# Kernel tuning notes

Measured on AMD Instinct MI355X. Metric: run time of the kernel, lower is better.

## Reference

```python
import jax, jax.numpy as jnp
import numpy as np

B, S, HID, NH = 64, 197, 768, 12
DH = HID // NH  # 64
EPS = 1e-24


def setup_inputs() -> dict:
    key = jax.random.key(0)
    ks = jax.random.split(key, 20)
    def lin(i):
        w = jax.random.normal(ks[i], (HID, HID), jnp.float32) * 0.02  # stored [in, out]
        b = jnp.zeros((HID,), jnp.float32)
        return w, b
    Wmq, bmq = lin(0); Wcq, bcq = lin(1)
    Wmk, bmk = lin(2); Wck, bck = lin(3)
    Wmv, bmv = lin(4); Wcv, bcv = lin(5)
    Wmd, bmd = lin(6); Wcd, bcd = lin(7)
    return dict(
        input_mean_tensor=jax.random.normal(ks[8], (B, S, HID), jnp.float32),
        input_cov_tensor=jax.random.normal(ks[9], (B, S, HID), jnp.float32),
        Wmq=Wmq, bmq=bmq, Wcq=Wcq, bcq=bcq,
        Wmk=Wmk, bmk=bmk, Wck=Wck, bck=bck,
        Wmv=Wmv, bmv=bmv, Wcv=Wcv, bcv=bcv,
        Wmd=Wmd, bmd=bmd, Wcd=Wcd, bcd=bcd,
    )


def _heads(x):
    # [B, S, HID] -> [B, NH, S, DH]
    return x.reshape(x.shape[0], x.shape[1], NH, DH).transpose(0, 2, 1, 3)


def _merge(x):
    # [B, NH, S, DH] -> [B, S, HID]
    return x.transpose(0, 2, 1, 3).reshape(x.shape[0], x.shape[2], HID)


def wasserstein_distance_matmul(m1, c1, m2, c2):
    # all [B, NH, S, DH]; returns [B, NH, S, S]
    m1_2 = jnp.sum(m1 * m1, -1, keepdims=True)            # [B,NH,S,1]
    m2_2 = jnp.sum(m2 * m2, -1, keepdims=True)
    ret = m1_2 + jnp.swapaxes(m2_2, -1, -2) - 2.0 * jnp.einsum('bhqd,bhkd->bhqk', m1, m2)
    c1_2 = jnp.sum(c1, -1, keepdims=True)
    c2_2 = jnp.sum(c2, -1, keepdims=True)
    s1 = jnp.sqrt(jnp.clip(c1, EPS, None))
    s2 = jnp.sqrt(jnp.clip(c2, EPS, None))
    cov_ret = c1_2 + jnp.swapaxes(c2_2, -1, -2) - 2.0 * jnp.einsum('bhqd,bhkd->bhqk', s1, s2)
    return ret + cov_ret


def reference(input_mean_tensor, input_cov_tensor,
              Wmq, bmq, Wcq, bcq, Wmk, bmk, Wck, bck,
              Wmv, bmv, Wcv, bcv, Wmd, bmd, Wcd, bcd):
    mean_q = _heads(input_mean_tensor @ Wmq + bmq)
    mean_k = _heads(input_mean_tensor @ Wmk + bmk)
    mean_v = _heads(input_mean_tensor @ Wmv + bmv)
    cov_q = _heads(jax.nn.elu(input_cov_tensor @ Wcq + bcq) + 1.0)
    cov_k = _heads(jax.nn.elu(input_cov_tensor @ Wck + bck) + 1.0)
    cov_v = _heads(jax.nn.elu(input_cov_tensor @ Wcv + bcv) + 1.0)

    scores = -wasserstein_distance_matmul(mean_q, cov_q, mean_k, cov_k)
    scores = scores / jnp.sqrt(jnp.float32(DH))
    probs = jax.nn.softmax(scores, axis=-1)  # [B,NH,S,S]

    mean_ctx = _merge(jnp.einsum('bhqk,bhkd->bhqd', probs, mean_v))
    cov_ctx = _merge(jnp.einsum('bhqk,bhkd->bhqd', probs * probs, cov_v))

    mean_hidden = mean_ctx @ Wmd + bmd
    cov_hidden = cov_ctx @ Wcd + bcd
    return (mean_hidden, cov_hidden)
```

## Files before the change

### kernel.cpp

```cpp
#include <hip/hip_runtime.h>
#include <hip/hip_bf16.h>
#include <stdint.h>

typedef _Float16 f16;
typedef _Float16 f16x8 __attribute__((ext_vector_type(8)));
typedef _Float16 f16x4 __attribute__((ext_vector_type(4)));
typedef float f32x4 __attribute__((ext_vector_type(4)));

constexpr int B = 64, S = 197, HID = 768, NH = 12, DH = 64;
constexpr int M = B * S;
constexpr int Mpad = 12800;
constexpr int BNS = B * NH * S;
constexpr int VSTRIDE = 224;
constexpr size_t NPH = (size_t)Mpad * HID;
constexpr size_t MH = (size_t)M * HID;
constexpr size_t WSZ1 = (size_t)HID * HID;
constexpr size_t VTSZ = (size_t)B * NH * DH * VSTRIDE;

__device__ __forceinline__ f32x4 mfma16(f16x8 a, f16x8 b, f32x4 c) {
  return __builtin_amdgcn_mfma_f32_16x16x32_f16(a, b, c, 0, 0, 0);
}

__device__ __forceinline__ void gload16(const void* g, void* l) {
  __builtin_amdgcn_global_load_lds(
      (const __attribute__((address_space(1))) void*)g,
      (__attribute__((address_space(3))) void*)l, 16, 0, 0);
}

__device__ __forceinline__ int xcd_swizzle(int wg, int nwg) {
  const int q = nwg >> 3, r = nwg & 7;
  const int x = wg & 7, p = wg >> 3;
  return (x < r ? x * (q + 1) : r * (q + 1) + (x - r) * q) + p;
}

__global__ __launch_bounds__(256) void zero_kernel(char* __restrict__ p, size_t n16) {
  const size_t i = (size_t)blockIdx.x * 256 + threadIdx.x;
  if (i < n16) reinterpret_cast<int4*>(p)[i] = int4{0, 0, 0, 0};
}

__global__ __launch_bounds__(256) void cvt_x_kernel(
    const float* __restrict__ xm, const float* __restrict__ xc,
    f16* __restrict__ ym, f16* __restrict__ yc) {
  const size_t i8 = ((size_t)blockIdx.x * 256 + threadIdx.x) * 8;
  f16x8 vm = {}, vc = {};
  if (i8 < MH) {
    const float4 a0 = *reinterpret_cast<const float4*>(xm + i8);
    const float4 a1 = *reinterpret_cast<const float4*>(xm + i8 + 4);
    const float4 b0 = *reinterpret_cast<const float4*>(xc + i8);
    const float4 b1 = *reinterpret_cast<const float4*>(xc + i8 + 4);
    vm[0] = (f16)a0.x; vm[1] = (f16)a0.y; vm[2] = (f16)a0.z; vm[3] = (f16)a0.w;
    vm[4] = (f16)a1.x; vm[5] = (f16)a1.y; vm[6] = (f16)a1.z; vm[7] = (f16)a1.w;
    vc[0] = (f16)b0.x; vc[1] = (f16)b0.y; vc[2] = (f16)b0.z; vc[3] = (f16)b0.w;
    vc[4] = (f16)b1.x; vc[5] = (f16)b1.y; vc[6] = (f16)b1.z; vc[7] = (f16)b1.w;
  }
  *reinterpret_cast<f16x8*>(ym + i8) = vm;
  *reinterpret_cast<f16x8*>(yc + i8) = vc;
}

struct WPtrs { const float* w[8]; };

__global__ __launch_bounds__(256) void cvt_w_kernel(WPtrs p, f16* __restrict__ wt) {
  __shared__ float tile[32][33];
  const int z = blockIdx.z;
  const float* W = p.w[z];
  f16* Wt = wt + (size_t)z * WSZ1;
  const int k0 = blockIdx.x * 32, n0 = blockIdx.y * 32;
  const int tx = threadIdx.x & 31, ty = threadIdx.x >> 5;
#pragma unroll
  for (int i = 0; i < 4; ++i)
    tile[ty + i * 8][tx] = W[(size_t)(k0 + ty + i * 8) * HID + n0 + tx];
  __syncthreads();
#pragma unroll
  for (int i = 0; i < 4; ++i)
    Wt[(size_t)(n0 + ty + i * 8) * HID + k0 + tx] = (f16)tile[tx][ty + i * 8];
}

__device__ __forceinline__ void gemm_core(
    const f16* __restrict__ Abase, const f16* __restrict__ Btbase,
    int m0, int n0, int tid, char (*lds)[32768], f32x4 (&acc)[8][4]) {
  const int w = tid >> 6, lane = tid & 63;
  const int l15 = lane & 15, lg = lane >> 4;
  const int wr = (w >> 2) * 128, wc = (w & 3) * 64;
  const int srow = w * 32 + (lane >> 3);
  const int scb = ((lane & 7) * 16) ^ ((srow & 7) << 4);
  const char* gA = reinterpret_cast<const char*>(Abase + (size_t)(m0 + srow) * HID) + scb;
  const char* gB = reinterpret_cast<const char*>(Btbase + (size_t)(n0 + srow) * HID) + scb;

#pragma unroll
  for (int i = 0; i < 4; ++i) {
    gload16(gA + (size_t)i * 8 * 1536, lds[0] + w * 4096 + i * 1024);
    gload16(gB + (size_t)i * 8 * 1536, lds[1] + w * 4096 + i * 1024);
  }

  int cur = 0;
  for (int kt = 0; kt < 12; ++kt) {
    if (kt + 1 < 12) {
      const size_t off = (size_t)(kt + 1) * 128;
#pragma unroll
      for (int i = 0; i < 4; ++i) {
        gload16(gA + off + (size_t)i * 8 * 1536, lds[2 - 2 * cur] + w * 4096 + i * 1024);
        gload16(gB + off + (size_t)i * 8 * 1536, lds[3 - 2 * cur] + w * 4096 + i * 1024);
      }
      asm volatile("s_waitcnt vmcnt(8)\n\ts_barrier" ::: "memory");
    } else {
      asm volatile("s_waitcnt vmcnt(0)\n\ts_barrier" ::: "memory");
    }
    const char* cA = lds[2 * cur];
    const char* cB = lds[2 * cur + 1];
#pragma unroll
    for (int ks = 0; ks < 2; ++ks) {
      f16x8 af[8], bf[4];
#pragma unroll
      for (int fi = 0; fi < 8; ++fi) {
        const int row = wr + l15 + fi * 16;
        af[fi] = *reinterpret_cast<const f16x8*>(
            cA + row * 128 + ((ks * 64 + lg * 16) ^ ((row & 7) << 4)));
      }
#pragma unroll
      for (int fj = 0; fj < 4; ++fj) {
        const int row = wc + l15 + fj * 16;
        bf[fj] = *reinterpret_cast<const f16x8*>(
            cB + row * 128 + ((ks * 64 + lg * 16) ^ ((row & 7) << 4)));
      }
#pragma unroll
      for (int fi = 0; fi < 8; ++fi)
#pragma unroll
        for (int fj = 0; fj < 4; ++fj)
          acc[fi][fj] = mfma16(af[fi], bf[fj], acc[fi][fj]);
    }
    asm volatile("s_waitcnt lgkmcnt(0)\n\ts_barrier" ::: "memory");
    cur ^= 1;
  }
}

struct ProjArgs {
  const f16* A[2]; const f16* Bt[2];
  const float* bias[2][3];
  f16* out0[2];
  f16* out1[2];
  f16* vt[2];
  float* qterm; float* kterm;
};

__global__ __launch_bounds__(512, 1) void gemm_proj(ProjArgs g) {
  __shared__ char lds[4][32768];
  const int swz = xcd_swizzle(blockIdx.x, 900);
  const int z = swz / 450;
  const int rest = swz - z * 450;
  const int x = rest / 9, y = rest - x * 9;
  const int m0 = x * 256, n0 = y * 256;

  f32x4 acc[8][4] = {};
  gemm_core(g.A[z], g.Bt[z], m0, n0, threadIdx.x, lds, acc);

  const int tid = threadIdx.x, w = tid >> 6, lane = tid & 63;
  const int l15 = lane & 15, lg = lane >> 4;
  const int wr = (w >> 2) * 128, wc = (w & 3) * 64;
  const int nsel = n0 / 768;
  const int colbase = (n0 - nsel * 768) + wc;
  const int rbase = m0 + wr + lg * 4;
  const float* bias = g.bias[z][nsel];
  const int hh = colbase >> 6;

  if (nsel < 2) {
    f16* Y = nsel ? g.out1[z] : g.out0[z];
    float* term = nsel ? g.kterm : g.qterm;
    float bv4[4];
#pragma unroll
    for (int fj = 0; fj < 4; ++fj) bv4[fj] = bias[colbase + l15 + fj * 16];
#pragma unroll
    for (int fi = 0; fi < 8; ++fi) {
#pragma unroll
      for (int r = 0; r < 4; ++r) {
        const int row = rbase + fi * 16 + r;
        float ssum = 0.f;
#pragma unroll
        for (int fj = 0; fj < 4; ++fj) {
          float v = acc[fi][fj][r] + bv4[fj];
          if (z == 1) { v = (v > 0.f) ? v + 1.f : __expf(v); v = sqrtf(v); }
          const f16 st = (f16)(v * 0.5f);
          if (row < M) Y[(size_t)row * HID + colbase + l15 + fj * 16] = st;
          const float sf = (float)st;
          ssum = fmaf(sf, sf, ssum);
        }
        ssum += __shfl_xor(ssum, 1, 64);
        ssum += __shfl_xor(ssum, 2, 64);
        ssum += __shfl_xor(ssum, 4, 64);
        ssum += __shfl_xor(ssum, 8, 64);
        if (l15 == 0 && row < M) {
          const int bb = row / S, ss = row - bb * S;
          atomicAdd(&term[(bb * NH + hh) * S + ss], 0.5f * ssum);
        }
      }
    }
  } else {
    f16* VT = g.vt[z];
#pragma unroll
    for (int fj = 0; fj < 4; ++fj) {
      const int col = colbase + l15 + fj * 16;
      const float bv = bias[col];
      const int dd = col & 63;
#pragma unroll
      for (int fi = 0; fi < 8; ++fi)
#pragma unroll
        for (int r = 0; r < 4; ++r) {
          const int row = rbase + fi * 16 + r;
          if (row < M) {
            float v = acc[fi][fj][r] + bv;
            if (z == 1) v = (v > 0.f) ? v + 1.f : __expf(v);
            const int bb = row / S, ss = row - bb * S;
            VT[((size_t)(bb * NH + hh) * DH + dd) * VSTRIDE + ss] = (f16)v;
          }
        }
    }
  }
}

struct OutArgs {
  const f16* A[2]; const f16* Bt[2]; const float* bias[2]; float* Y[2];
};

__global__ __launch_bounds__(512, 1) void gemm_out(OutArgs g) {
  __shared__ char lds[4][32768];
  const int swz = xcd_swizzle(blockIdx.x, 300);
  const int z = swz / 150;
  const int rest = swz - z * 150;
  const int x = rest / 3, y = rest - x * 3;
  const int m0 = x * 256, n0 = y * 256;

  f32x4 acc[8][4] = {};
  gemm_core(g.A[z], g.Bt[z], m0, n0, threadIdx.x, lds, acc);

  const int tid = threadIdx.x, w = tid >> 6, lane = tid & 63;
  const int l15 = lane & 15, lg = lane >> 4;
  const int wr = (w >> 2) * 128, wc = (w & 3) * 64;
  const int rbase = m0 + wr + lg * 4;
  float* Y = g.Y[z];
#pragma unroll
  for (int fj = 0; fj < 4; ++fj) {
    const int col = n0 + wc + l15 + fj * 16;
    const float bv = g.bias[z][col];
#pragma unroll
    for (int fi = 0; fi < 8; ++fi)
#pragma unroll
      for (int r = 0; r < 4; ++r) {
        const int row = rbase + fi * 16 + r;
        if (row < M) Y[(size_t)row * HID + col] = acc[fi][fj][r] + bv;
      }
  }
}

__global__ __launch_bounds__(256, 2) void attn_kernel(
    const f16* __restrict__ mq, const f16* __restrict__ sq,
    const f16* __restrict__ mk, const f16* __restrict__ sk,
    const f16* __restrict__ vtm, const f16* __restrict__ vtc,
    const float* __restrict__ qterm, const float* __restrict__ kterm,
    f16* __restrict__ mean_ctx, f16* __restrict__ cov_ctx) {
  __shared__ char Pb[64 * 512];
  __shared__ float qt_s[64];
  __shared__ float kt_s[256];
  __shared__ float red_m[4][64];
  __shared__ float red_s[4][64];

  const int swz = xcd_swizzle(blockIdx.x, 3072);
  const int qtile = swz & 3, bh = swz >> 2;
  const int h = bh % NH, b = bh / NH;
  const int s0 = qtile * 64;
  const int tid = threadIdx.x, w = tid >> 6, lane = tid & 63;
  const int l15 = lane & 15, lg = lane >> 4;

  const size_t base = (size_t)(b * S) * HID + (size_t)h * DH;
  const int tb = bh * S;

  f16x8 qmf[4][2], qsf[4][2];
#pragma unroll
  for (int fi = 0; fi < 4; ++fi) {
    const size_t o = base + (size_t)(s0 + fi * 16 + l15) * HID + lg * 8;
    qmf[fi][0] = *reinterpret_cast<const f16x8*>(mq + o);
    qmf[fi][1] = *reinterpret_cast<const f16x8*>(mq + o + 32);
    qsf[fi][0] = *reinterpret_cast<const f16x8*>(sq + o);
    qsf[fi][1] = *reinterpret_cast<const f16x8*>(sq + o + 32);
  }
  if (tid < 64) qt_s[tid] = (s0 + tid < S) ? qterm[tb + s0 + tid] : 0.f;
  kt_s[tid] = (tid < S) ? kterm[tb + tid] : 0.f;
  __syncthreads();

  f32x4 acc[4][4] = {};
  __builtin_amdgcn_s_setprio(1);
#pragma unroll
  for (int fj = 0; fj < 4; ++fj) {
    const size_t o = base + (size_t)(w * 64 + fj * 16 + l15) * HID + lg * 8;
    const f16x8 a0 = *reinterpret_cast<const f16x8*>(mk + o);
    const f16x8 a1 = *reinterpret_cast<const f16x8*>(mk + o + 32);
    const f16x8 c0 = *reinterpret_cast<const f16x8*>(sk + o);
    const f16x8 c1 = *reinterpret_cast<const f16x8*>(sk + o + 32);
#pragma unroll
    for (int fi = 0; fi < 4; ++fi) {
      acc[fj][fi] = mfma16(a0, qmf[fi][0], acc[fj][fi]);
      acc[fj][fi] = mfma16(c0, qsf[fi][0], acc[fj][fi]);
      acc[fj][fi] = mfma16(a1, qmf[fi][1], acc[fj][fi]);
      acc[fj][fi] = mfma16(c1, qsf[fi][1], acc[fj][fi]);
    }
  }
  __builtin_amdgcn_s_setprio(0);

  const int d = w * 16 + l15;
  const size_t vbase = ((size_t)bh * DH + d) * VSTRIDE + lg * 8;
  f16x8 vmr[7], vcr[7];
#pragma unroll
  for (int ks = 0; ks < 7; ++ks) {
    vmr[ks] = *reinterpret_cast<const f16x8*>(vtm + vbase + ks * 32);
    vcr[ks] = *reinterpret_cast<const f16x8*>(vtc + vbase + ks * 32);
  }

#pragma unroll
  for (int fi = 0; fi < 4; ++fi) {
    const float qv = qt_s[fi * 16 + l15];
    float mx = -1e30f;
#pragma unroll
    for (int fj = 0; fj < 4; ++fj)
#pragma unroll
      for (int r = 0; r < 4; ++r) {
        const int j = w * 64 + fj * 16 + lg * 4 + r;
        float sv = acc[fj][fi][r] - qv - kt_s[j];
        if (j >= S) sv = -1e30f;
        acc[fj][fi][r] = sv;
        mx = fmaxf(mx, sv);
      }
    mx = fmaxf(mx, __shfl_xor(mx, 16, 64));
    mx = fmaxf(mx, __shfl_xor(mx, 32, 64));
    if (lg == 0) red_m[w][fi * 16 + l15] = mx;
  }
  __syncthreads();

#pragma unroll
  for (int fi = 0; fi < 4; ++fi) {
    const int q = fi * 16 + l15;
    const float m = fmaxf(fmaxf(red_m[0][q], red_m[1][q]),
                          fmaxf(red_m[2][q], red_m[3][q]));
    const int xr = (q & 7) << 4;
    float sum = 0.f;
#pragma unroll
    for (int fj = 0; fj < 4; ++fj) {
      f16x4 p4;
#pragma unroll
      for (int r = 0; r < 4; ++r) {
        const float e = __expf(acc[fj][fi][r] - m);
        sum += e;
        p4[r] = (f16)e;
      }
      *reinterpret_cast<f16x4*>(
          Pb + q * 512 + ((2 * (w * 64 + fj * 16 + lg * 4)) ^ xr)) = p4;
    }
    sum += __shfl_xor(sum, 16, 64);
    sum += __shfl_xor(sum, 32, 64);
    if (lg == 0) red_s[w][q] = sum;
  }
  __syncthreads();

  f32x4 macc[4] = {}, cacc[4] = {};
  __builtin_amdgcn_s_setprio(1);
#pragma unroll
  for (int ks = 0; ks < 7; ++ks) {
#pragma unroll
    for (int fi = 0; fi < 4; ++fi) {
      const int q = fi * 16 + l15;
      const f16x8 pa = *reinterpret_cast<const f16x8*>(
          Pb + q * 512 + ((2 * (ks * 32 + lg * 8)) ^ ((q & 7) << 4)));
      macc[fi] = mfma16(pa, vmr[ks], macc[fi]);
      const f16x8 pq = pa * pa;
      cacc[fi] = mfma16(pq, vcr[ks], cacc[fi]);
    }
  }
  __builtin_amdgcn_s_setprio(0);

#pragma unroll
  for (int fi = 0; fi < 4; ++fi)
#pragma unroll
    for (int r = 0; r < 4; ++r) {
      const int qo = fi * 16 + lg * 4 + r;
      const int srow = s0 + qo;
      if (srow < S) {
        const float tot = red_s[0][qo] + red_s[1][qo] + red_s[2][qo] + red_s[3][qo];
        const float inv = 1.f / tot;
        const size_t oidx = (size_t)(b * S + srow) * HID + h * DH + d;
        mean_ctx[oidx] = (f16)(macc[fi][r] * inv);
        cov_ctx[oidx] = (f16)(cacc[fi][r] * inv * inv);
      }
    }
}

extern "C" void kernel_launch(void* const* d_in, const int* in_sizes, int n_in,
                              void* d_out, int out_size, void* d_ws, size_t ws_size,
                              hipStream_t stream) {
  const float* in_mean = (const float*)d_in[0];
  const float* in_cov = (const float*)d_in[1];
  const float* Wmq = (const float*)d_in[2];  const float* bmq = (const float*)d_in[3];
  const float* Wcq = (const float*)d_in[4];  const float* bcq = (const float*)d_in[5];
  const float* Wmk = (const float*)d_in[6];  const float* bmk = (const float*)d_in[7];
  const float* Wck = (const float*)d_in[8];  const float* bck = (const float*)d_in[9];
  const float* Wmv = (const float*)d_in[10]; const float* bmv = (const float*)d_in[11];
  const float* Wcv = (const float*)d_in[12]; const float* bcv = (const float*)d_in[13];
  const float* Wmd = (const float*)d_in[14]; const float* bmd = (const float*)d_in[15];
  const float* Wcd = (const float*)d_in[16]; const float* bcd = (const float*)d_in[17];

  const size_t need = (2 * NPH + 8 * WSZ1 + 4 * MH + 2 * VTSZ) * sizeof(f16) +
                      2 * (size_t)BNS * sizeof(float);
  if (ws_size < need) return;

  f16* Xm = (f16*)d_ws;
  f16* Xc = Xm + NPH;
  f16* Wt = Xc + NPH;
  f16* mq = Wt + 8 * WSZ1;
  f16* mk = mq + MH;
  f16* sq = mk + MH;
  f16* sk = sq + MH;
  f16* vtm = sk + MH;
  f16* vtc = vtm + VTSZ;
  float* qterm = (float*)(vtc + VTSZ);
  float* kterm = qterm + BNS;
  f16* mean_ctx = Xm;
  f16* cov_ctx = Xc;

  float* out_mean = (float*)d_out;
  float* out_cov = out_mean + MH;

  dim3 blk(256);

  const size_t zbytes = 2 * VTSZ * sizeof(f16) + 2 * (size_t)BNS * sizeof(float);
  const size_t n16 = zbytes / 16;
  zero_kernel<<<(int)((n16 + 255) / 256), blk, 0, stream>>>((char*)vtm, n16);

  cvt_x_kernel<<<(int)(NPH / 2048), blk, 0, stream>>>(in_mean, in_cov, Xm, Xc);

  WPtrs wp;
  wp.w[0] = Wmq; wp.w[1] = Wmk; wp.w[2] = Wmv;
  wp.w[3] = Wcq; wp.w[4] = Wck; wp.w[5] = Wcv;
  wp.w[6] = Wmd; wp.w[7] = Wcd;
  cvt_w_kernel<<<dim3(24, 24, 8), blk, 0, stream>>>(wp, Wt);

  ProjArgs pa;
  pa.A[0] = Xm; pa.A[1] = Xc;
  pa.Bt[0] = Wt; pa.Bt[1] = Wt + 3 * WSZ1;
  pa.bias[0][0] = bmq; pa.bias[0][1] = bmk; pa.bias[0][2] = bmv;
  pa.bias[1][0] = bcq; pa.bias[1][1] = bck; pa.bias[1][2] = bcv;
  pa.out0[0] = mq; pa.out0[1] = sq;
  pa.out1[0] = mk; pa.out1[1] = sk;
  pa.vt[0] = vtm; pa.vt[1] = vtc;
  pa.qterm = qterm; pa.kterm = kterm;
  gemm_proj<<<900, dim3(512), 0, stream>>>(pa);

  attn_kernel<<<3072, blk, 0, stream>>>(mq, sq, mk, sk, vtm, vtc,
                                        qterm, kterm, mean_ctx, cov_ctx);

  OutArgs oa;
  oa.A[0] = mean_ctx; oa.A[1] = cov_ctx;
  oa.Bt[0] = Wt + 6 * WSZ1; oa.Bt[1] = Wt + 7 * WSZ1;
  oa.bias[0] = bmd; oa.bias[1] = bcd;
  oa.Y[0] = out_mean; oa.Y[1] = out_cov;
  gemm_out<<<300, dim3(512), 0, stream>>>(oa);
}
```

Before: 381.0 us.

## Switch GEMM core to 3-stage LDS pipeline with BK=32 and MFMA priority

```diff
diff --git a/kernel.cpp b/kernel.cpp
--- a/kernel.cpp
+++ b/kernel.cpp
@@ -77,60 +77,61 @@
 
 __device__ __forceinline__ void gemm_core(
     const f16* __restrict__ Abase, const f16* __restrict__ Btbase,
-    int m0, int n0, int tid, char (*lds)[32768], f32x4 (&acc)[8][4]) {
+    int m0, int n0, int tid, char* lds, f32x4 (&acc)[8][4]) {
   const int w = tid >> 6, lane = tid & 63;
   const int l15 = lane & 15, lg = lane >> 4;
   const int wr = (w >> 2) * 128, wc = (w & 3) * 64;
-  const int srow = w * 32 + (lane >> 3);
-  const int scb = ((lane & 7) * 16) ^ ((srow & 7) << 4);
-  const char* gA = reinterpret_cast<const char*>(Abase + (size_t)(m0 + srow) * HID) + scb;
-  const char* gB = reinterpret_cast<const char*>(Btbase + (size_t)(n0 + srow) * HID) + scb;
-
-#pragma unroll
-  for (int i = 0; i < 4; ++i) {
-    gload16(gA + (size_t)i * 8 * 1536, lds[0] + w * 4096 + i * 1024);
-    gload16(gB + (size_t)i * 8 * 1536, lds[1] + w * 4096 + i * 1024);
-  }
-
-  int cur = 0;
-  for (int kt = 0; kt < 12; ++kt) {
-    if (kt + 1 < 12) {
-      const size_t off = (size_t)(kt + 1) * 128;
-#pragma unroll
-      for (int i = 0; i < 4; ++i) {
-        gload16(gA + off + (size_t)i * 8 * 1536, lds[2 - 2 * cur] + w * 4096 + i * 1024);
-        gload16(gB + off + (size_t)i * 8 * 1536, lds[3 - 2 * cur] + w * 4096 + i * 1024);
-      }
-      asm volatile("s_waitcnt vmcnt(8)\n\ts_barrier" ::: "memory");
-    } else {
+
+  const int srow = w * 32 + (lane >> 2);
+  const int scol = (lane & 3) * 16;
+  const char* gA = reinterpret_cast<const char*>(Abase + (size_t)(m0 + srow) * HID) + scol;
+  const char* gB = reinterpret_cast<const char*>(Btbase + (size_t)(n0 + srow) * HID) + scol;
+  const int wbase = w * 2048;
+
+#define STAGE_TILE(T, BUF)                                               \
+  do {                                                                   \
+    const size_t off_ = (size_t)(T) * 64;                                \
+    char* la_ = lds + (BUF) * 32768 + wbase;                             \
+    char* lb_ = la_ + 16384;                                             \
+    gload16(gA + off_, la_);                                             \
+    gload16(gA + off_ + (size_t)16 * 1536, la_ + 1024);                  \
+    gload16(gB + off_, lb_);                                             \
+    gload16(gB + off_ + (size_t)16 * 1536, lb_ + 1024);                  \
+  } while (0)
+
+  STAGE_TILE(0, 0);
+  STAGE_TILE(1, 1);
+  asm volatile("s_waitcnt vmcnt(4)\n\ts_barrier" ::: "memory");
+
+#pragma unroll
+  for (int t = 0; t < 24; ++t) {
+    if (t + 2 < 24) STAGE_TILE(t + 2, (t + 2) % 3);
+
+    const char* cA = lds + (t % 3) * 32768;
+    const char* cB = cA + 16384;
+    f16x8 af[8], bf[4];
+#pragma unroll
+    for (int fi = 0; fi < 8; ++fi)
+      af[fi] = *reinterpret_cast<const f16x8*>(cA + (wr + l15 + fi * 16) * 64 + lg * 16);
+#pragma unroll
+    for (int fj = 0; fj < 4; ++fj)
+      bf[fj] = *reinterpret_cast<const f16x8*>(cB + (wc + l15 + fj * 16) * 64 + lg * 16);
+
+    __builtin_amdgcn_s_setprio(1);
+#pragma unroll
+    for (int fi = 0; fi < 8; ++fi)
+#pragma unroll
+      for (int fj = 0; fj < 4; ++fj)
+        acc[fi][fj] = mfma16(af[fi], bf[fj], acc[fi][fj]);
+    __builtin_amdgcn_s_setprio(0);
+
+    if (t + 2 < 24) {
+      asm volatile("s_waitcnt vmcnt(4)\n\ts_barrier" ::: "memory");
+    } else if (t + 1 < 24) {
       asm volatile("s_waitcnt vmcnt(0)\n\ts_barrier" ::: "memory");
     }
-    const char* cA = lds[2 * cur];
-    const char* cB = lds[2 * cur + 1];
-#pragma unroll
-    for (int ks = 0; ks < 2; ++ks) {
-      f16x8 af[8], bf[4];
-#pragma unroll
-      for (int fi = 0; fi < 8; ++fi) {
-        const int row = wr + l15 + fi * 16;
-        af[fi] = *reinterpret_cast<const f16x8*>(
-            cA + row * 128 + ((ks * 64 + lg * 16) ^ ((row & 7) << 4)));
-      }
-#pragma unroll
-      for (int fj = 0; fj < 4; ++fj) {
-        const int row = wc + l15 + fj * 16;
-        bf[fj] = *reinterpret_cast<const f16x8*>(
-            cB + row * 128 + ((ks * 64 + lg * 16) ^ ((row & 7) << 4)));
-      }
-#pragma unroll
-      for (int fi = 0; fi < 8; ++fi)
-#pragma unroll
-        for (int fj = 0; fj < 4; ++fj)
-          acc[fi][fj] = mfma16(af[fi], bf[fj], acc[fi][fj]);
-    }
-    asm volatile("s_waitcnt lgkmcnt(0)\n\ts_barrier" ::: "memory");
-    cur ^= 1;
-  }
+  }
+#undef STAGE_TILE
 }
 
 struct ProjArgs {
@@ -143,7 +144,7 @@
 };
 
 __global__ __launch_bounds__(512, 1) void gemm_proj(ProjArgs g) {
-  __shared__ char lds[4][32768];
+  __shared__ alignas(16) char lds[98304];
   const int swz = xcd_swizzle(blockIdx.x, 900);
   const int z = swz / 450;
   const int rest = swz - z * 450;
@@ -221,7 +222,7 @@
 };
 
 __global__ __launch_bounds__(512, 1) void gemm_out(OutArgs g) {
-  __shared__ char lds[4][32768];
+  __shared__ alignas(16) char lds[98304];
   const int swz = xcd_swizzle(blockIdx.x, 300);
   const int z = swz / 150;
   const int rest = swz - z * 150;
```

Result: no change. 376.4 us (-1.2%).
